# Kernel tuning notes

Measured on AMD Instinct MI355X. Metric: run time of the kernel, lower is better.

## Reference

```python
import jax, jax.numpy as jnp
import numpy as np

TAO = 1.0
EPS = 1e-8


def setup_inputs() -> dict:
    key = jax.random.key(0)
    k1, k2, k3 = jax.random.split(key, 3)
    B, S, H = 32, 64, 256
    tmap = jax.random.normal(k1, (B, S, S, H), dtype=jnp.float32)
    pos_query = jax.random.normal(k2, (B, H), dtype=jnp.float32)
    r = jax.random.uniform(k3, (B, S, S))
    mask2d_pos = r < 0.05
    mask2d_neg = (r >= 0.05) & (r < 0.35)
    return {"pos_query": pos_query, "tmap": tmap,
            "mask2d_pos": mask2d_pos, "mask2d_neg": mask2d_neg}


def reference(pos_query, tmap, mask2d_pos, mask2d_neg):
    # Original loops over batch, gathers variable-length pos/neg sets, normalizes
    # twice (once without eps, once with eps inside sim()), then InfoNCE-style loss.
    # Vectorized: compute similarities for ALL (i,j) cells once, reduce with masks.
    u = tmap / jnp.linalg.norm(tmap, axis=-1, keepdims=True)          # pos/neg normalize (no eps)
    u = u / (jnp.linalg.norm(u, axis=-1, keepdims=True) + EPS)        # renormalize inside sim() (with eps)
    q = pos_query / (jnp.linalg.norm(pos_query, axis=-1, keepdims=True) + EPS)
    s = jnp.einsum('bijh,bh->bij', u, q)                              # cosine sims (B,S,S)
    e = jnp.exp(s / TAO)
    num = jnp.sum(e * mask2d_pos, axis=(1, 2))                        # sum exp(pos_sim/tao)
    den = num + jnp.sum(e * mask2d_neg, axis=(1, 2))                  # + sum exp(neg_sim/tao)
    li = -jnp.log(num / (den + EPS))                                  # per-sample loss (B,)
    # original skips samples with empty pos or neg set, averages over the rest
    valid = jnp.any(mask2d_pos, axis=(1, 2)) & jnp.any(mask2d_neg, axis=(1, 2))
    n_valid = jnp.maximum(jnp.sum(valid), 1)
    return jnp.sum(jnp.where(valid, li, 0.0)) / n_valid
```

## Files before the change

### kernel.cpp

```cpp
#include <hip/hip_runtime.h>
#include <math.h>

#define EPSF 1e-8f
constexpr int B = 32;
constexpr int S = 64;
constexpr int H = 256;
constexpr int H4 = H / 4;
constexpr int CELLS_PER_BATCH = S * S;
constexpr int CELLS = B * CELLS_PER_BATCH;
constexpr int CELLS_PER_WAVE = 8;
constexpr int WAVES_PER_BLOCK = 4;
constexpr int CELLS_PER_BLOCK = CELLS_PER_WAVE * WAVES_PER_BLOCK;

#define WS_ACC_BASE 64
#define WS_ACC_STRIDE 32
#define WS_NEG_OFF 16

__global__ __launch_bounds__(64) void prep_kernel(const float* __restrict__ pq,
                                                  float* __restrict__ ws) {
    int b = blockIdx.x;
    int lane = threadIdx.x;
    float4 v = ((const float4*)pq)[b * H4 + lane];
    float ss = v.x * v.x + v.y * v.y + v.z * v.z + v.w * v.w;
    #pragma unroll
    for (int off = 32; off > 0; off >>= 1) ss += __shfl_xor(ss, off);
    if (lane == 0) {
        ws[b] = 1.0f / (sqrtf(ss) + EPSF);
        ws[WS_ACC_BASE + b * WS_ACC_STRIDE] = 0.0f;
        ws[WS_ACC_BASE + b * WS_ACC_STRIDE + WS_NEG_OFF] = 0.0f;
    }
}

__global__ __launch_bounds__(256) void main_kernel(const float* __restrict__ tmap,
                                                   const float* __restrict__ pq,
                                                   const int* __restrict__ mask_pos,
                                                   const int* __restrict__ mask_neg,
                                                   float* __restrict__ ws) {
    int tid = threadIdx.x;
    int lane = tid & 63;
    int wid = tid >> 6;
    int cellBase = blockIdx.x * CELLS_PER_BLOCK + wid * CELLS_PER_WAVE;
    int b = cellBase >> 12;

    float4 q4 = ((const float4*)pq)[b * H4 + lane];
    float scale = ws[b] * (1.0f / (1.0f + EPSF));

    float wp = 0.0f, wn = 0.0f;
    #pragma unroll
    for (int k = 0; k < CELLS_PER_WAVE; ++k) {
        int cell = cellBase + k;
        float4 t = ((const float4*)tmap)[cell * H4 + lane];
        float d  = t.x * q4.x + t.y * q4.y + t.z * q4.z + t.w * q4.w;
        float ss = t.x * t.x + t.y * t.y + t.z * t.z + t.w * t.w;
        #pragma unroll
        for (int off = 32; off > 0; off >>= 1) {
            d  += __shfl_xor(d, off);
            ss += __shfl_xor(ss, off);
        }
        float s = d * scale * rsqrtf(ss);
        float e = __expf(s);
        if (mask_pos[cell] != 0) wp += e;
        if (mask_neg[cell] != 0) wn += e;
    }

    __shared__ float sp[WAVES_PER_BLOCK], sn[WAVES_PER_BLOCK];
    if (lane == 0) { sp[wid] = wp; sn[wid] = wn; }
    __syncthreads();
    if (tid == 0) {
        float tp = 0.0f, tn = 0.0f;
        #pragma unroll
        for (int w = 0; w < WAVES_PER_BLOCK; ++w) { tp += sp[w]; tn += sn[w]; }
        atomicAdd(&ws[WS_ACC_BASE + b * WS_ACC_STRIDE], tp);
        atomicAdd(&ws[WS_ACC_BASE + b * WS_ACC_STRIDE + WS_NEG_OFF], tn);
    }
}

__global__ __launch_bounds__(64) void final_kernel(const float* __restrict__ ws,
                                                   float* __restrict__ out) {
    int lane = threadIdx.x;
    float li = 0.0f;
    int v = 0;
    if (lane < B) {
        float ep = ws[WS_ACC_BASE + lane * WS_ACC_STRIDE];
        float en = ws[WS_ACC_BASE + lane * WS_ACC_STRIDE + WS_NEG_OFF];
        if (ep > 0.0f && en > 0.0f) {
            v = 1;
            li = -logf(ep / (ep + en + EPSF));
        }
    }
    #pragma unroll
    for (int off = 32; off > 0; off >>= 1) {
        li += __shfl_xor(li, off);
        v  += __shfl_xor(v, off);
    }
    if (lane == 0) out[0] = li / (float)(v > 0 ? v : 1);
}

extern "C" void kernel_launch(void* const* d_in, const int* in_sizes, int n_in,
                              void* d_out, int out_size, void* d_ws, size_t ws_size,
                              hipStream_t stream) {
    const float* pos_query = (const float*)d_in[0];
    const float* tmap      = (const float*)d_in[1];
    const int*   mask_pos  = (const int*)d_in[2];
    const int*   mask_neg  = (const int*)d_in[3];
    float* out = (float*)d_out;
    float* ws  = (float*)d_ws;

    prep_kernel<<<B, 64, 0, stream>>>(pos_query, ws);
    main_kernel<<<CELLS / CELLS_PER_BLOCK, 256, 0, stream>>>(tmap, pos_query,
                                                             mask_pos, mask_neg, ws);
    final_kernel<<<1, 64, 0, stream>>>(ws, out);
}
```

Baseline: 195.8 us.

## Skip tmap loads for cells outside both masks using wave ballots

Each wave now loads its cell masks up front, ballots the positive and negative bits, and iterates only over cells where either mask is set. It loads the next active cell's row while computing the current one. Cells per wave double to 16. This avoids reading tmap rows that cannot contribute to the loss, cutting HBM traffic. The trade-off is a data-dependent loop with only single-step prefetch, which may lower memory-level parallelism per wave.

```diff
diff --git a/kernel.cpp b/kernel.cpp
--- a/kernel.cpp
+++ b/kernel.cpp
@@ -8,7 +8,7 @@
 constexpr int H4 = H / 4;
 constexpr int CELLS_PER_BATCH = S * S;
 constexpr int CELLS = B * CELLS_PER_BATCH;
-constexpr int CELLS_PER_WAVE = 8;
+constexpr int CELLS_PER_WAVE = 16;
 constexpr int WAVES_PER_BLOCK = 4;
 constexpr int CELLS_PER_BLOCK = CELLS_PER_WAVE * WAVES_PER_BLOCK;
 
@@ -45,22 +45,44 @@
     float4 q4 = ((const float4*)pq)[b * H4 + lane];
     float scale = ws[b] * (1.0f / (1.0f + EPSF));
 
+    int mp = 0, mn = 0;
+    if (lane < CELLS_PER_WAVE) {
+        mp = mask_pos[cellBase + lane];
+        mn = mask_neg[cellBase + lane];
+    }
+    unsigned long long bp = __ballot(mp != 0);
+    unsigned long long bn = __ballot(mn != 0);
+    unsigned long long act = bp | bn;
+
     float wp = 0.0f, wn = 0.0f;
-    #pragma unroll
-    for (int k = 0; k < CELLS_PER_WAVE; ++k) {
-        int cell = cellBase + k;
-        float4 t = ((const float4*)tmap)[cell * H4 + lane];
-        float d  = t.x * q4.x + t.y * q4.y + t.z * q4.z + t.w * q4.w;
-        float ss = t.x * t.x + t.y * t.y + t.z * t.z + t.w * t.w;
-        #pragma unroll
-        for (int off = 32; off > 0; off >>= 1) {
-            d  += __shfl_xor(d, off);
-            ss += __shfl_xor(ss, off);
+
+    if (act) {
+        const float4* t4 = (const float4*)tmap;
+        int k = __ffsll(act) - 1;
+        unsigned long long rem = act & (act - 1);
+        float4 t = t4[(cellBase + k) * H4 + lane];
+        for (;;) {
+            int kn = -1;
+            float4 tnext;
+            if (rem) {
+                kn = __ffsll(rem) - 1;
+                rem &= rem - 1;
+                tnext = t4[(cellBase + kn) * H4 + lane];
+            }
+            float d  = t.x * q4.x + t.y * q4.y + t.z * q4.z + t.w * q4.w;
+            float ss = t.x * t.x + t.y * t.y + t.z * t.z + t.w * t.w;
+            #pragma unroll
+            for (int off = 32; off > 0; off >>= 1) {
+                d  += __shfl_xor(d, off);
+                ss += __shfl_xor(ss, off);
+            }
+            float s = d * scale * rsqrtf(ss);
+            float e = __expf(s);
+            if ((bp >> k) & 1) wp += e;
+            if ((bn >> k) & 1) wn += e;
+            if (kn < 0) break;
+            k = kn; t = tnext;
         }
-        float s = d * scale * rsqrtf(ss);
-        float e = __expf(s);
-        if (mask_pos[cell] != 0) wp += e;
-        if (mask_neg[cell] != 0) wn += e;
     }
 
     __shared__ float sp[WAVES_PER_BLOCK], sn[WAVES_PER_BLOCK];
```

Measured after the change: 187.6 us. 1.04x faster.
